# Kernel tuning notes

Hardware: AMD Instinct MI355X
Metric: run time of the kernel (lower is better)

## Reference

```python
import jax, jax.numpy as jnp
import numpy as np

N_HEADS = 4
D_K = 64


def setup_inputs() -> dict:
    key = jax.random.key(0)
    k1, k2, k3, k4, k5 = jax.random.split(key, 5)
    C = 256
    return {
        "x": jax.random.normal(k1, (16, C, 32, 32), dtype=jnp.float32),
        "W_qkv": jax.random.normal(k2, (C, N_HEADS * D_K * 3), dtype=jnp.float32) * (C ** -0.5),
        "b_qkv": jax.random.normal(k3, (N_HEADS * D_K * 3,), dtype=jnp.float32) * 0.02,
        "W_out": jax.random.normal(k4, (N_HEADS * D_K, C), dtype=jnp.float32) * ((N_HEADS * D_K) ** -0.5),
        "b_out": jax.random.normal(k5, (C,), dtype=jnp.float32) * 0.02,
    }


def reference(x, W_qkv, b_qkv, W_out, b_out):
    # NOTE: the original forward never applies self.norm and ignores t.
    B, C, H, W = x.shape
    N = H * W
    scale = D_K ** -0.5
    xf = x.reshape(B, C, N).transpose(0, 2, 1)            # [B, N, C]
    qkv = (xf @ W_qkv + b_qkv).reshape(B, N, N_HEADS, 3 * D_K)
    q, k, v = jnp.split(qkv, 3, axis=-1)                  # each [B, N, H, dk]
    attn = jnp.einsum('bihd,bjhd->bijh', q, k) * scale    # [B, N, N, H]
    attn = jax.nn.softmax(attn, axis=2)                   # softmax over keys (j)
    res = jnp.einsum('bijh,bjhd->bihd', attn, v)          # [B, N, H, dk]
    res = res.reshape(B, N, N_HEADS * D_K)
    res = res @ W_out + b_out + xf                        # residual on flattened x
    return res.transpose(0, 2, 1).reshape(B, C, H, W)
```

## Files before the change

kernel.cpp:

```cpp
#include <hip/hip_runtime.h>
#include <math.h>

#define NN 1024

typedef __attribute__((ext_vector_type(8))) __bf16 bf16x8;
typedef __attribute__((ext_vector_type(4))) __bf16 bf16x4;
typedef __attribute__((ext_vector_type(4))) short s16x4;
typedef __attribute__((ext_vector_type(4))) float f32x4;

__device__ __forceinline__ unsigned short f2bf(float f) {
    __bf16 h = (__bf16)f;
    return *(unsigned short*)&h;
}
__device__ __forceinline__ ushort4 pack4(float a, float b, float c, float d) {
    bf16x4 v;
    v[0] = (__bf16)a; v[1] = (__bf16)b; v[2] = (__bf16)c; v[3] = (__bf16)d;
    return *(ushort4*)&v;
}
__device__ __forceinline__ float bf2f(unsigned short u) {
    unsigned v = (unsigned)u << 16;
    return __uint_as_float(v);
}

__device__ __forceinline__ f32x4 mfma16x16x16(ushort4 a, ushort4 b, f32x4 c) {
#if __has_builtin(__builtin_amdgcn_mfma_f32_16x16x16_bf16)
    return __builtin_amdgcn_mfma_f32_16x16x16_bf16(
        *(bf16x4*)&a, *(bf16x4*)&b, c, 0, 0, 0);
#else
    return __builtin_amdgcn_mfma_f32_16x16x16bf16_1k(
        *(s16x4*)&a, *(s16x4*)&b, c, 0, 0, 0);
#endif
}

__device__ __forceinline__ void async_cp16(const unsigned short* g, unsigned short* l) {
    __builtin_amdgcn_global_load_lds(
        (const __attribute__((address_space(1))) unsigned int*)g,
        (__attribute__((address_space(3))) unsigned int*)l,
        16, 0, 0);
}

__global__ __launch_bounds__(256) void prep_transpose(
    const float* __restrict__ x, const float* __restrict__ Wq,
    const float* __restrict__ Wo,
    unsigned short* __restrict__ xb, unsigned short* __restrict__ Wqt,
    unsigned short* __restrict__ Wot)
{
    __shared__ __align__(16) unsigned short T[64 * 72];
    const int bx = blockIdx.x;
    const int rt = blockIdx.y;
    const float* src; unsigned short* dst; int ncol, c0;
    if (bx < 256) {
        int b = bx >> 4; int ct = bx & 15;
        src = x + (size_t)b * 256 * 1024; dst = xb + (size_t)b * 1024 * 256;
        ncol = 1024; c0 = ct * 64;
    } else if (bx < 268) {
        src = Wq; dst = Wqt; ncol = 768; c0 = (bx - 256) * 64;
    } else {
        src = Wo; dst = Wot; ncol = 256; c0 = (bx - 268) * 64;
    }
    const int t = threadIdx.x;
    #pragma unroll
    for (int i = 0; i < 4; ++i) {
        int r  = i * 16 + (t >> 4);
        int c4 = (t & 15) * 4;
        float4 v = *(const float4*)&src[(size_t)(rt * 64 + r) * ncol + c0 + c4];
        *(ushort4*)&T[r * 72 + c4] = pack4(v.x, v.y, v.z, v.w);
    }
    __syncthreads();
    #pragma unroll
    for (int i = 0; i < 2; ++i) {
        int task = t + 256 * i;
        int c = task & 63, rs = task >> 6;
        ushort u8[8];
        #pragma unroll
        for (int k = 0; k < 8; ++k) u8[k] = T[(rs * 8 + k) * 72 + c];
        *(uint4*)&dst[(size_t)(c0 + c) * 256 + rt * 64 + rs * 8] = *(uint4*)u8;
    }
}

__global__ __launch_bounds__(256, 2) void qkv_gemm(
    const unsigned short* __restrict__ xb, const unsigned short* __restrict__ Wqt,
    const float* __restrict__ bias,
    unsigned short* __restrict__ Qb, unsigned short* __restrict__ Kb,
    unsigned short* __restrict__ Vtb)
{
    __shared__ __align__(16) unsigned short As[2][8192];
    __shared__ __align__(16) unsigned short Bs[2][8192];
    const int jt = blockIdx.x;
    const int m0 = blockIdx.y * 128;
    const int b  = m0 >> 10;
    const int n0 = m0 & 1023;
    const int t = threadIdx.x;
    const int w = t >> 6, lane = t & 63, quad = lane >> 4, cc = lane & 15;
    const int wm = (w & 1) * 64;
    const int wj = (w >> 1) * 64;

    f32x4 acc[4][4];
    #pragma unroll
    for (int ms = 0; ms < 4; ++ms)
        #pragma unroll
        for (int js = 0; js < 4; ++js) acc[ms][js] = (f32x4)(0.f);

    auto stage = [&](int k0, unsigned short* dA, unsigned short* dB) {
        #pragma unroll
        for (int i = 0; i < 4; ++i) {
            int f = i * 256 + t;
            int row = f >> 3;
            int gc  = (f & 7) ^ (row & 7);
            async_cp16(&xb[(size_t)(m0 + row) * 256 + k0 + gc * 8], &dA[f * 8]);
            async_cp16(&Wqt[(size_t)(jt * 128 + row) * 256 + k0 + gc * 8], &dB[f * 8]);
        }
    };

    stage(0, As[0], Bs[0]);
    __syncthreads();

    #pragma unroll
    for (int s = 0; s < 4; ++s) {
        const int cur = s & 1;
        if (s > 0) __syncthreads();
        if (s < 3) stage((s + 1) * 64, As[cur ^ 1], Bs[cur ^ 1]);

        #pragma unroll
        for (int ks = 0; ks < 2; ++ks) {
            bf16x8 af[4], bfr[4];
            #pragma unroll
            for (int ms = 0; ms < 4; ++ms) {
                int row = wm + ms * 16 + cc;
                int sc = (ks * 4 + quad) ^ (cc & 7);
                af[ms] = *(bf16x8*)&As[cur][row * 64 + sc * 8];
            }
            #pragma unroll
            for (int js = 0; js < 4; ++js) {
                int row = wj + js * 16 + cc;
                int sc = (ks * 4 + quad) ^ (cc & 7);
                bfr[js] = *(bf16x8*)&Bs[cur][row * 64 + sc * 8];
            }
            #pragma unroll
            for (int ms = 0; ms < 4; ++ms)
                #pragma unroll
                for (int js = 0; js < 4; ++js)
                    acc[ms][js] = __builtin_amdgcn_mfma_f32_16x16x32_bf16(
                        af[ms], bfr[js], acc[ms][js], 0, 0, 0);
        }
    }

    const int chunk = jt * 2 + (w >> 1);
    const int h = chunk / 3, type = chunk % 3;
    const size_t bh = (size_t)b * 4 + h;
    float bias_r[4];
    #pragma unroll
    for (int js = 0; js < 4; ++js) bias_r[js] = bias[jt * 128 + wj + js * 16 + cc];

    if (type == 2) {
        #pragma unroll
        for (int ms = 0; ms < 4; ++ms)
            #pragma unroll
            for (int js = 0; js < 4; ++js) {
                int dd = js * 16 + cc;
                int n = n0 + wm + ms * 16 + quad * 4;
                *(ushort4*)&Vtb[(bh * 64 + dd) * NN + n] =
                    pack4(acc[ms][js][0] + bias_r[js], acc[ms][js][1] + bias_r[js],
                          acc[ms][js][2] + bias_r[js], acc[ms][js][3] + bias_r[js]);
            }
    } else {
        unsigned short* dst = type ? Kb : Qb;
        const float sc = type ? 1.0f : 0.18033688011112042f;
        #pragma unroll
        for (int ms = 0; ms < 4; ++ms)
            #pragma unroll
            for (int js = 0; js < 4; ++js)
                #pragma unroll
                for (int r = 0; r < 4; ++r) {
                    int n = n0 + wm + ms * 16 + quad * 4 + r;
                    dst[(bh * NN + n) * 64 + js * 16 + cc] =
                        f2bf((acc[ms][js][r] + bias_r[js]) * sc);
                }
    }
}

__global__ __launch_bounds__(256, 4) void flash_attn(
    const unsigned short* __restrict__ Qb, const unsigned short* __restrict__ Kb,
    const unsigned short* __restrict__ Vtb, unsigned short* __restrict__ resb)
{
    __shared__ __align__(16) unsigned short Ks0[4096];
    __shared__ __align__(16) unsigned short Ks1[4096];
    __shared__ __align__(16) unsigned short Vt0[4096];
    __shared__ __align__(16) unsigned short Vt1[4096];

    const int blk = blockIdx.x;
    const int qt = blk & 15;
    const int h  = (blk >> 4) & 3;
    const int b  = blk >> 6;
    const int t  = threadIdx.x;
    const int w  = t >> 6;
    const int lane = t & 63;
    const int quad = lane >> 4;
    const int c    = lane & 15;

    const size_t bh = (size_t)(b * 4 + h);
    const unsigned short* Qg = Qb  + bh * NN * 64;
    const unsigned short* Kg = Kb  + bh * NN * 64;
    const unsigned short* Vg = Vtb + bh * 64 * NN;

    #pragma unroll
    for (int i = 0; i < 2; ++i) {
        int f = i * 256 + t;
        int row = f >> 3;
        int gc  = (f & 7) ^ (row & 7);
        async_cp16(&Kg[(size_t)row * 64 + gc * 8], &Ks0[f * 8]);
        async_cp16(&Vg[(size_t)row * NN + gc * 8], &Vt0[f * 8]);
    }
    bf16x8 qf[2];
    #pragma unroll
    for (int ks = 0; ks < 2; ++ks)
        qf[ks] = *(const bf16x8*)&Qg[(size_t)(qt * 64 + w * 16 + c) * 64 +
                                     ks * 32 + quad * 8];
    __syncthreads();

    float l_part = 0.f;
    f32x4 O[4];
    #pragma unroll
    for (int dt = 0; dt < 4; ++dt) O[dt] = (f32x4)(0.f);

    auto step = [&](int kt, const unsigned short* curK, const unsigned short* curV,
                    unsigned short* nxtK, unsigned short* nxtV,
                    bool pref, bool bar) {
        if (bar) __syncthreads();
        if (pref) {
            int ktn = kt + 1;
            #pragma unroll
            for (int i = 0; i < 2; ++i) {
                int f = i * 256 + t;
                int row = f >> 3;
                int gc  = (f & 7) ^ (row & 7);
                async_cp16(&Kg[(size_t)(ktn * 64 + row) * 64 + gc * 8], &nxtK[f * 8]);
                async_cp16(&Vg[(size_t)row * NN + ktn * 64 + gc * 8], &nxtV[f * 8]);
            }
        }

        f32x4 S[4];
        #pragma unroll
        for (int jt = 0; jt < 4; ++jt) S[jt] = (f32x4)(0.f);
        #pragma unroll
        for (int ks = 0; ks < 2; ++ks) {
            #pragma unroll
            for (int jt = 0; jt < 4; ++jt) {
                int sc_ = (ks * 4 + quad) ^ (c & 7);
                bf16x8 kf = *(bf16x8*)&curK[((jt * 16 + c) * 8 + sc_) * 8];
                S[jt] = __builtin_amdgcn_mfma_f32_16x16x32_bf16(kf, qf[ks], S[jt], 0, 0, 0);
            }
        }

        ushort4 Pf[4];
        #pragma unroll
        for (int jt = 0; jt < 4; ++jt) {
            float p0 = __builtin_amdgcn_exp2f(S[jt][0]);
            float p1 = __builtin_amdgcn_exp2f(S[jt][1]);
            float p2 = __builtin_amdgcn_exp2f(S[jt][2]);
            float p3 = __builtin_amdgcn_exp2f(S[jt][3]);
            l_part += (p0 + p1) + (p2 + p3);
            Pf[jt] = pack4(p0, p1, p2, p3);
        }

        #pragma unroll
        for (int jt = 0; jt < 4; ++jt) {
            #pragma unroll
            for (int dt = 0; dt < 4; ++dt) {
                int sc_ = (jt * 2 + (quad >> 1)) ^ (c & 7);
                ushort4 vfrag = *(ushort4*)&curV[(dt * 16 + c) * 64 +
                                                 sc_ * 8 + (quad & 1) * 4];
                O[dt] = mfma16x16x16(Pf[jt], vfrag, O[dt]);
            }
        }
    };

    step(0, Ks0, Vt0, Ks1, Vt1, true, false);
    for (int kt2 = 0; kt2 < 7; ++kt2) {
        int kt = 2 * kt2 + 1;
        step(kt,     Ks1, Vt1, Ks0, Vt0, true, true);
        step(kt + 1, Ks0, Vt0, Ks1, Vt1, true, true);
    }
    step(15, Ks1, Vt1, Ks0, Vt0, false, true);

    float l_tot = l_part;
    l_tot += __shfl_xor(l_tot, 16);
    l_tot += __shfl_xor(l_tot, 32);

    float linv[4];
    #pragma unroll
    for (int r = 0; r < 4; ++r) linv[r] = 1.f / __shfl(l_tot, quad * 4 + r);
    #pragma unroll
    for (int dt = 0; dt < 4; ++dt)
        #pragma unroll
        for (int r = 0; r < 4; ++r) {
            int row = qt * 64 + w * 16 + quad * 4 + r;
            resb[((size_t)(b * NN + row)) * 256 + h * 64 + dt * 16 + c] =
                f2bf(O[dt][r] * linv[r]);
        }
}

__global__ __launch_bounds__(256, 4) void out_gemm(
    const unsigned short* __restrict__ resb, const unsigned short* __restrict__ Wot,
    const float* __restrict__ bias, const unsigned short* __restrict__ xb,
    float* __restrict__ out)
{
    __shared__ __align__(16) unsigned short As[2][4096];
    __shared__ __align__(16) unsigned short Bs[2][4096];
    const int n0 = blockIdx.x * 64;
    const int c0 = blockIdx.y * 64;
    const int b  = blockIdx.z;
    const int t = threadIdx.x;
    const int w = t >> 6, lane = t & 63, quad = lane >> 4, cc = lane & 15;
    const int wm = (w & 1) * 32;
    const int wj = (w >> 1) * 32;

    f32x4 acc[2][2];
    #pragma unroll
    for (int ms = 0; ms < 2; ++ms)
        #pragma unroll
        for (int js = 0; js < 2; ++js) acc[ms][js] = (f32x4)(0.f);

    auto stage = [&](int k0, unsigned short* dA, unsigned short* dB) {
        #pragma unroll
        for (int i = 0; i < 2; ++i) {
            int f = i * 256 + t;
            int row = f >> 3;
            int gc  = (f & 7) ^ (row & 7);
            async_cp16(&resb[((size_t)b * NN + n0 + row) * 256 + k0 + gc * 8], &dA[f * 8]);
            async_cp16(&Wot[(size_t)(c0 + row) * 256 + k0 + gc * 8], &dB[f * 8]);
        }
    };

    stage(0, As[0], Bs[0]);
    __syncthreads();

    #pragma unroll
    for (int s = 0; s < 4; ++s) {
        const int cur = s & 1;
        if (s > 0) __syncthreads();
        if (s < 3) stage((s + 1) * 64, As[cur ^ 1], Bs[cur ^ 1]);

        #pragma unroll
        for (int ks = 0; ks < 2; ++ks) {
            bf16x8 af[2], bfr[2];
            #pragma unroll
            for (int ms = 0; ms < 2; ++ms) {
                int row = wm + ms * 16 + cc;
                int sc = (ks * 4 + quad) ^ (cc & 7);
                af[ms] = *(bf16x8*)&As[cur][row * 64 + sc * 8];
            }
            #pragma unroll
            for (int js = 0; js < 2; ++js) {
                int row = wj + js * 16 + cc;
                int sc = (ks * 4 + quad) ^ (cc & 7);
                bfr[js] = *(bf16x8*)&Bs[cur][row * 64 + sc * 8];
            }
            #pragma unroll
            for (int ms = 0; ms < 2; ++ms)
                #pragma unroll
                for (int js = 0; js < 2; ++js)
                    acc[ms][js] = __builtin_amdgcn_mfma_f32_16x16x32_bf16(
                        af[ms], bfr[js], acc[ms][js], 0, 0, 0);
        }
    }

    #pragma unroll
    for (int js = 0; js < 2; ++js) {
        int cI = c0 + wj + js * 16 + cc;
        float bi = bias[cI];
        #pragma unroll
        for (int ms = 0; ms < 2; ++ms) {
            int n = n0 + wm + ms * 16 + quad * 4;
            size_t off = ((size_t)b * 256 + cI) * NN + n;
            float4 o;
            float* op = &o.x;
            #pragma unroll
            for (int r = 0; r < 4; ++r) {
                float xr = bf2f(xb[((size_t)b * NN + n + r) * 256 + cI]);
                op[r] = acc[ms][js][r] + bi + xr;
            }
            *(float4*)&out[off] = o;
        }
    }
}

extern "C" void kernel_launch(void* const* d_in, const int* in_sizes, int n_in,
                              void* d_out, int out_size, void* d_ws, size_t ws_size,
                              hipStream_t stream)
{
    const float* x     = (const float*)d_in[0];
    const float* W_qkv = (const float*)d_in[1];
    const float* b_qkv = (const float*)d_in[2];
    const float* W_out = (const float*)d_in[3];
    const float* b_out = (const float*)d_in[4];
    float* out = (float*)d_out;

    char* wsc = (char*)d_ws;
    unsigned short* xb   = (unsigned short*)(wsc);
    unsigned short* Wqt  = (unsigned short*)(wsc + ((size_t)8 << 20));
    unsigned short* Wot  = (unsigned short*)(wsc + ((size_t)8 << 20) + ((size_t)512 << 10));
    unsigned short* Qb   = (unsigned short*)(wsc + ((size_t)9  << 20));
    unsigned short* Kb   = (unsigned short*)(wsc + ((size_t)17 << 20));
    unsigned short* Vtb  = (unsigned short*)(wsc + ((size_t)25 << 20));
    unsigned short* resb = (unsigned short*)(wsc + ((size_t)33 << 20));

    prep_transpose<<<dim3(272, 4), 256, 0, stream>>>(x, W_qkv, W_out, xb, Wqt, Wot);
    qkv_gemm<<<dim3(6, 128), 256, 0, stream>>>(xb, Wqt, b_qkv, Qb, Kb, Vtb);
    flash_attn<<<dim3(1024), 256, 0, stream>>>(Qb, Kb, Vtb, resb);
    out_gemm<<<dim3(16, 4, 16), 256, 0, stream>>>(resb, Wot, b_out, xb, out);
}
```

Before: 131.0 us.

## Split attention key tiles across waves and reduce partial outputs in LDS

```diff
diff --git a/kernel.cpp b/kernel.cpp
--- a/kernel.cpp
+++ b/kernel.cpp
@@ -179,14 +179,15 @@
     }
 }
 
-__global__ __launch_bounds__(256, 4) void flash_attn(
+__global__ __launch_bounds__(256, 3) void flash_attn(
     const unsigned short* __restrict__ Qb, const unsigned short* __restrict__ Kb,
     const unsigned short* __restrict__ Vtb, unsigned short* __restrict__ resb)
 {
-    __shared__ __align__(16) unsigned short Ks0[4096];
-    __shared__ __align__(16) unsigned short Ks1[4096];
-    __shared__ __align__(16) unsigned short Vt0[4096];
-    __shared__ __align__(16) unsigned short Vt1[4096];
+    __shared__ __align__(16) unsigned short LDS[16384];
+    unsigned short* Ks0 = LDS;
+    unsigned short* Ks1 = LDS + 4096;
+    unsigned short* Vt0 = LDS + 8192;
+    unsigned short* Vt1 = LDS + 12288;
 
     const int blk = blockIdx.x;
     const int qt = blk & 15;
@@ -211,17 +212,21 @@
         async_cp16(&Kg[(size_t)row * 64 + gc * 8], &Ks0[f * 8]);
         async_cp16(&Vg[(size_t)row * NN + gc * 8], &Vt0[f * 8]);
     }
-    bf16x8 qf[2];
-    #pragma unroll
-    for (int ks = 0; ks < 2; ++ks)
-        qf[ks] = *(const bf16x8*)&Qg[(size_t)(qt * 64 + w * 16 + c) * 64 +
-                                     ks * 32 + quad * 8];
+    bf16x8 qf[4][2];
+    #pragma unroll
+    for (int mt = 0; mt < 4; ++mt)
+        #pragma unroll
+        for (int ks = 0; ks < 2; ++ks)
+            qf[mt][ks] = *(const bf16x8*)&Qg[(size_t)(qt * 64 + mt * 16 + c) * 64 +
+                                             ks * 32 + quad * 8];
     __syncthreads();
 
-    float l_part = 0.f;
-    f32x4 O[4];
-    #pragma unroll
-    for (int dt = 0; dt < 4; ++dt) O[dt] = (f32x4)(0.f);
+    float l_part[4] = {0.f, 0.f, 0.f, 0.f};
+    f32x4 O[4][4];
+    #pragma unroll
+    for (int mt = 0; mt < 4; ++mt)
+        #pragma unroll
+        for (int dt = 0; dt < 4; ++dt) O[mt][dt] = (f32x4)(0.f);
 
     auto step = [&](int kt, const unsigned short* curK, const unsigned short* curV,
                     unsigned short* nxtK, unsigned short* nxtV,
@@ -239,39 +244,35 @@
             }
         }
 
-        f32x4 S[4];
-        #pragma unroll
-        for (int jt = 0; jt < 4; ++jt) S[jt] = (f32x4)(0.f);
+        bf16x8 kf[2];
         #pragma unroll
         for (int ks = 0; ks < 2; ++ks) {
-            #pragma unroll
-            for (int jt = 0; jt < 4; ++jt) {
-                int sc_ = (ks * 4 + quad) ^ (c & 7);
-                bf16x8 kf = *(bf16x8*)&curK[((jt * 16 + c) * 8 + sc_) * 8];
-                S[jt] = __builtin_amdgcn_mfma_f32_16x16x32_bf16(kf, qf[ks], S[jt], 0, 0, 0);
-            }
+            int sc_ = (ks * 4 + quad) ^ (c & 7);
+            kf[ks] = *(bf16x8*)&curK[((w * 16 + c) * 8 + sc_) * 8];
         }
 
         ushort4 Pf[4];
         #pragma unroll
-        for (int jt = 0; jt < 4; ++jt) {
-            float p0 = __builtin_amdgcn_exp2f(S[jt][0]);
-            float p1 = __builtin_amdgcn_exp2f(S[jt][1]);
-            float p2 = __builtin_amdgcn_exp2f(S[jt][2]);
-            float p3 = __builtin_amdgcn_exp2f(S[jt][3]);
-            l_part += (p0 + p1) + (p2 + p3);
-            Pf[jt] = pack4(p0, p1, p2, p3);
-        }
-
-        #pragma unroll
-        for (int jt = 0; jt < 4; ++jt) {
-            #pragma unroll
-            for (int dt = 0; dt < 4; ++dt) {
-                int sc_ = (jt * 2 + (quad >> 1)) ^ (c & 7);
-                ushort4 vfrag = *(ushort4*)&curV[(dt * 16 + c) * 64 +
-                                                 sc_ * 8 + (quad & 1) * 4];
-                O[dt] = mfma16x16x16(Pf[jt], vfrag, O[dt]);
-            }
+        for (int mt = 0; mt < 4; ++mt) {
+            f32x4 S = (f32x4)(0.f);
+            S = __builtin_amdgcn_mfma_f32_16x16x32_bf16(kf[0], qf[mt][0], S, 0, 0, 0);
+            S = __builtin_amdgcn_mfma_f32_16x16x32_bf16(kf[1], qf[mt][1], S, 0, 0, 0);
+            float p0 = __builtin_amdgcn_exp2f(S[0]);
+            float p1 = __builtin_amdgcn_exp2f(S[1]);
+            float p2 = __builtin_amdgcn_exp2f(S[2]);
+            float p3 = __builtin_amdgcn_exp2f(S[3]);
+            l_part[mt] += (p0 + p1) + (p2 + p3);
+            Pf[mt] = pack4(p0, p1, p2, p3);
+        }
+
+        int scv = (w * 2 + (quad >> 1)) ^ (c & 7);
+        #pragma unroll
+        for (int dt = 0; dt < 4; ++dt) {
+            ushort4 vfrag = *(ushort4*)&curV[(dt * 16 + c) * 64 +
+                                             scv * 8 + (quad & 1) * 4];
+            #pragma unroll
+            for (int mt = 0; mt < 4; ++mt)
+                O[mt][dt] = mfma16x16x16(Pf[mt], vfrag, O[mt][dt]);
         }
     };
 
@@ -283,21 +284,49 @@
     }
     step(15, Ks1, Vt1, Ks0, Vt0, false, true);
 
-    float l_tot = l_part;
-    l_tot += __shfl_xor(l_tot, 16);
-    l_tot += __shfl_xor(l_tot, 32);
-
-    float linv[4];
-    #pragma unroll
-    for (int r = 0; r < 4; ++r) linv[r] = 1.f / __shfl(l_tot, quad * 4 + r);
-    #pragma unroll
-    for (int dt = 0; dt < 4; ++dt)
-        #pragma unroll
-        for (int r = 0; r < 4; ++r) {
-            int row = qt * 64 + w * 16 + quad * 4 + r;
-            resb[((size_t)(b * NN + row)) * 256 + h * 64 + dt * 16 + c] =
-                f2bf(O[dt][r] * linv[r]);
-        }
+    #pragma unroll
+    for (int mt = 0; mt < 4; ++mt) {
+        l_part[mt] += __shfl_xor(l_part[mt], 16);
+        l_part[mt] += __shfl_xor(l_part[mt], 32);
+    }
+
+    __syncthreads();
+    float* Osum = (float*)LDS;
+    float* Lsum = (float*)LDS + 64 * 68;
+    #pragma unroll
+    for (int ph = 0; ph < 4; ++ph) {
+        if (w == ph) {
+            #pragma unroll
+            for (int mt = 0; mt < 4; ++mt) {
+                #pragma unroll
+                for (int dt = 0; dt < 4; ++dt)
+                    #pragma unroll
+                    for (int r = 0; r < 4; ++r) {
+                        float* p = &Osum[(mt * 16 + quad * 4 + r) * 68 + dt * 16 + c];
+                        if (ph == 0) *p = O[mt][dt][r];
+                        else         *p += O[mt][dt][r];
+                    }
+                if (quad == 0) {
+                    float* lp = &Lsum[mt * 16 + c];
+                    if (ph == 0) *lp = l_part[mt];
+                    else         *lp += l_part[mt];
+                }
+            }
+        }
+        __syncthreads();
+    }
+
+    #pragma unroll
+    for (int r = 0; r < 4; ++r) {
+        int mrow = w * 16 + quad * 4 + r;
+        float linv = 1.f / Lsum[mrow];
+        #pragma unroll
+        for (int dt = 0; dt < 4; ++dt) {
+            float o = Osum[mrow * 68 + dt * 16 + c];
+            resb[((size_t)(b * NN + qt * 64 + mrow)) * 256 + h * 64 + dt * 16 + c] =
+                f2bf(o * linv);
+        }
+    }
 }
 
 __global__ __launch_bounds__(256, 4) void out_gemm(
```

After: 137.0 us. +4.6%, slower.
